# Kernel optimization log

Hardware: AMD Instinct MI355X
Metric: run time of the kernel (lower is better)

Reference implementation:

```python
import jax, jax.numpy as jnp
import numpy as np

NB = 8      # number of diagonal blocks per layer
BIN = 512   # in-block size
BOUT = 512  # out-block size


def setup_inputs() -> dict:
    key = jax.random.key(0)
    k_x, k_w1, k_b1, k_w2, k_b2 = jax.random.split(key, 5)
    B, D = 8192, NB * BIN
    x = jax.random.normal(k_x, (B, D), dtype=jnp.float32)
    # Block-diagonal weights stored as stacked blocks [NB, out_blk, in_blk]
    s1 = 1.0 / np.sqrt(BIN)
    W1 = jax.random.uniform(k_w1, (NB, BOUT, BIN), jnp.float32, -s1, s1)
    b1 = jax.random.uniform(k_b1, (NB * BOUT,), jnp.float32, -s1, s1)
    s2 = 1.0 / np.sqrt(BIN)
    W2 = jax.random.uniform(k_w2, (NB, BOUT, BIN), jnp.float32, -s2, s2)
    b2 = jax.random.uniform(k_b2, (NB * BOUT,), jnp.float32, -s2, s2)
    return {"x": x, "W1": W1, "b1": b1, "W2": W2, "b2": b2}


def _blockdiag_linear(x, W, b):
    # x: [B, NB*BIN]; W: [NB, BOUT, BIN]; b: [NB*BOUT]
    B = x.shape[0]
    xb = x.reshape(B, NB, BIN)                      # [B, NB, BIN]
    yb = jnp.einsum('bnc,noc->bno', xb, W)          # block-diag matmul
    return yb.reshape(B, NB * W.shape[1]) + b


def reference(x, W1, b1, W2, b2):
    x = x.reshape(x.shape[0], -1)                   # flatten(start_dim=1)
    h = jax.nn.relu(_blockdiag_linear(x, W1, b1))
    out = jax.nn.relu(_blockdiag_linear(h, W2, b2))
    return out
```

## Files before the change

kernel.cpp:

```cpp
#include <hip/hip_runtime.h>
#include <hip/hip_bf16.h>

#define NB 8
#define BIN 512
#define BOUT 512
#define BATCH 8192
#define DIM 4096

typedef __attribute__((ext_vector_type(8))) short bf16x8;
typedef __attribute__((ext_vector_type(4))) float f32x4;

#define SWZ(r) (((r) & 7) << 4)

__device__ __forceinline__ unsigned short f2bf(float f) {
    return __builtin_bit_cast(unsigned short, __float2bfloat16(f));
}

__device__ __forceinline__ unsigned long long pack4(f32x4 f) {
    return (unsigned long long)f2bf(f.x)
         | ((unsigned long long)f2bf(f.y) << 16)
         | ((unsigned long long)f2bf(f.z) << 32)
         | ((unsigned long long)f2bf(f.w) << 48);
}

__global__ void pack_w(const float* __restrict__ W, unsigned short* __restrict__ pk) {
    int gid = blockIdx.x * 256 + threadIdx.x;
    int lane = gid & 63;
    int n    = (gid >> 6) & 7;
    int kidx = (gid >> 9) & 15;
    int wn   = (gid >> 13) & 3;
    int nb   = gid >> 15;
    int row  = wn * 128 + n * 16 + (lane & 15);
    int col  = kidx * 32 + (lane >> 4) * 8;
    const float* s = W + ((size_t)nb * BOUT + row) * BIN + col;
    f32x4 a = *(const f32x4*)s;
    f32x4 b = *(const f32x4*)(s + 4);
    unsigned long long* d = (unsigned long long*)(pk + (size_t)gid * 8);
    d[0] = pack4(a);
    d[1] = pack4(b);
}

__global__ __launch_bounds__(256, 2)
void fused_mlp(const float* __restrict__ X,
               const unsigned short* __restrict__ PK1,
               const float* __restrict__ B1,
               const unsigned short* __restrict__ PK2,
               const float* __restrict__ B2,
               float* __restrict__ Out)
{
    __shared__ __align__(16) unsigned char LB[65536];

    const int bid = blockIdx.x;
    const int nb = bid & 7;
    const int mt = bid >> 3;

    const int t = threadIdx.x;
    const int lane = t & 63;
    const int wn = t >> 6;
    const int l15 = lane & 15;
    const int lhi = lane >> 4;

    const int row0 = mt * 64;
    const int wc0  = nb * 512;

    int ab[4][2];
    #pragma unroll
    for (int m = 0; m < 4; m++) {
        const int r_ = m * 16 + l15;
        #pragma unroll
        for (int par = 0; par < 2; par++)
            ab[m][par] = r_ * 1024 + ((par * 64 + lhi * 16) ^ SWZ(r_));
    }

    const unsigned short* wp1 = PK1 + (size_t)(nb * 4 + wn) * 65536 + lane * 8;
    const unsigned short* wp2 = PK2 + (size_t)(nb * 4 + wn) * 65536 + lane * 8;

    f32x4 acc[4][8];
    #pragma unroll
    for (int m = 0; m < 4; m++)
        #pragma unroll
        for (int n = 0; n < 8; n++)
            acc[m][n] = (f32x4)(0.f);

    bf16x8 q0[8], q1[8];

#define LOADQ(Q, WPTR) { \
    _Pragma("unroll") for (int n = 0; n < 8; n++) \
        Q[n] = *(const bf16x8*)((WPTR) + n * 512); \
    (WPTR) += 4096; }

#define MFMA32(Q, AF) \
    __builtin_amdgcn_s_setprio(1); \
    _Pragma("unroll") for (int m = 0; m < 4; m++) \
        _Pragma("unroll") for (int n = 0; n < 8; n++) \
            acc[m][n] = __builtin_amdgcn_mfma_f32_16x16x32_bf16(AF[m], Q[n], acc[m][n], 0, 0, 0); \
    __builtin_amdgcn_s_setprio(0);

#define HSTEP(QC, QN, WPTR, KIDX) { \
    LOADQ(QN, WPTR); \
    bf16x8 af[4]; \
    _Pragma("unroll") for (int m = 0; m < 4; m++) \
        af[m] = *(const bf16x8*)(LB + ab[m][(KIDX) & 1] + ((KIDX) >> 1) * 128); \
    MFMA32(QC, af) }

#define HSTEP_NL(QC, KIDX) { \
    bf16x8 af[4]; \
    _Pragma("unroll") for (int m = 0; m < 4; m++) \
        af[m] = *(const bf16x8*)(LB + ab[m][(KIDX) & 1] + ((KIDX) >> 1) * 128); \
    MFMA32(QC, af) }

#define BAR() { \
    asm volatile("s_waitcnt lgkmcnt(0)" ::: "memory"); \
    __builtin_amdgcn_s_barrier(); \
    __builtin_amdgcn_sched_barrier(0); }

    LOADQ(q0, wp1);

    {
        const int sr = t >> 2;
        const float* xr = X + (size_t)(row0 + sr) * DIM + wc0 + (t & 3) * 128;
        const int j0 = (t & 3) * 16;
        #pragma unroll
        for (int i = 0; i < 8; i++) {
            f32x4 a = *(const f32x4*)(xr + i * 16 + 0);
            f32x4 b = *(const f32x4*)(xr + i * 16 + 4);
            f32x4 c = *(const f32x4*)(xr + i * 16 + 8);
            f32x4 d = *(const f32x4*)(xr + i * 16 + 12);
            bf16x8 v0, v1;
            ((unsigned long long*)&v0)[0] = pack4(a);
            ((unsigned long long*)&v0)[1] = pack4(b);
            ((unsigned long long*)&v1)[0] = pack4(c);
            ((unsigned long long*)&v1)[1] = pack4(d);
            *(bf16x8*)(LB + sr * 1024 + (((j0 + 2 * i)     * 16) ^ SWZ(sr))) = v0;
            *(bf16x8*)(LB + sr * 1024 + (((j0 + 2 * i + 1) * 16) ^ SWZ(sr))) = v1;
        }
    }
    BAR();

    #pragma unroll
    for (int kp = 0; kp < 8; kp++) {
        HSTEP(q0, q1, wp1, 2 * kp);
        if (kp < 7) { HSTEP(q1, q0, wp1, 2 * kp + 1) }
        else        { HSTEP(q1, q0, wp2, 15)         }
    }

    BAR();

    #pragma unroll
    for (int n = 0; n < 8; n++) {
        const int c = wn * 128 + n * 16 + l15;
        const float bv = B1[wc0 + c];
        #pragma unroll
        for (int m = 0; m < 4; m++) {
            #pragma unroll
            for (int rr = 0; rr < 4; rr++) {
                float v = acc[m][n][rr] + bv;
                v = v > 0.f ? v : 0.f;
                const int r = m * 16 + lhi * 4 + rr;
                *(unsigned short*)(LB + r * 1024 + ((c * 2) ^ SWZ(r))) = f2bf(v);
            }
        }
    }
    BAR();

    #pragma unroll
    for (int m = 0; m < 4; m++)
        #pragma unroll
        for (int n = 0; n < 8; n++)
            acc[m][n] = (f32x4)(0.f);

    #pragma unroll
    for (int kp = 0; kp < 8; kp++) {
        HSTEP(q0, q1, wp2, 2 * kp);
        if (kp < 7) { HSTEP(q1, q0, wp2, 2 * kp + 1) }
        else        { HSTEP_NL(q1, 15) }
    }

    #pragma unroll
    for (int n = 0; n < 8; n++) {
        const int c = wc0 + wn * 128 + n * 16 + l15;
        const float bv = B2[c];
        #pragma unroll
        for (int m = 0; m < 4; m++) {
            const int rb = row0 + m * 16 + lhi * 4;
            #pragma unroll
            for (int rr = 0; rr < 4; rr++) {
                float v = acc[m][n][rr] + bv;
                Out[(size_t)(rb + rr) * DIM + c] = v > 0.f ? v : 0.f;
            }
        }
    }

#undef LOADQ
#undef MFMA32
#undef HSTEP
#undef HSTEP_NL
#undef BAR
}

extern "C" void kernel_launch(void* const* d_in, const int* in_sizes, int n_in,
                              void* d_out, int out_size, void* d_ws, size_t ws_size,
                              hipStream_t stream) {
    const float* x  = (const float*)d_in[0];
    const float* W1 = (const float*)d_in[1];
    const float* b1 = (const float*)d_in[2];
    const float* W2 = (const float*)d_in[3];
    const float* b2 = (const float*)d_in[4];
    float* out = (float*)d_out;

    char* ws = (char*)d_ws;
    unsigned short* PK1 = (unsigned short*)ws;
    unsigned short* PK2 = (unsigned short*)(ws + (4u << 20));

    pack_w<<<1024, 256, 0, stream>>>(W1, PK1);
    pack_w<<<1024, 256, 0, stream>>>(W2, PK2);

    const int GRID = NB * (BATCH / 64);
    fused_mlp<<<GRID, 256, 0, stream>>>(x, PK1, b1, PK2, b2, out);
}
```

Baseline: 101.5 us.

## Stage packed weights through triple-buffered LDS ring via async global_load_lds with 8 waves

Replaces per-wave register streaming of packed bf16 weights with a block-shared triple-buffered LDS ring filled by global_load_lds, synchronised by a vmcnt wait and barrier each k-step. The block grows to 512 threads with each wave owning 64 output columns, the weight packing layout is reordered to match, the X swizzle is widened to 16 rows, and biases are preloaded. The aim is to overlap weight fetch with MFMA work and cut register pressure. In exchange it adds a barrier per step, more A-fragment LDS reads per MFMA, and 160KB of LDS per block.

```diff
diff --git a/kernel.cpp b/kernel.cpp
--- a/kernel.cpp
+++ b/kernel.cpp
@@ -10,7 +10,7 @@
 typedef __attribute__((ext_vector_type(8))) short bf16x8;
 typedef __attribute__((ext_vector_type(4))) float f32x4;
 
-#define SWZ(r) (((r) & 7) << 4)
+#define SWZ16(r) (((r) & 15) << 4)
 
 __device__ __forceinline__ unsigned short f2bf(float f) {
     return __builtin_bit_cast(unsigned short, __float2bfloat16(f));
@@ -23,15 +23,21 @@
          | ((unsigned long long)f2bf(f.w) << 48);
 }
 
+__device__ __forceinline__ void gload16(const void* g, void* l) {
+    __builtin_amdgcn_global_load_lds(
+        (const __attribute__((address_space(1))) unsigned int*)g,
+        (__attribute__((address_space(3))) unsigned int*)l, 16, 0, 0);
+}
+
 __global__ void pack_w(const float* __restrict__ W, unsigned short* __restrict__ pk) {
     int gid = blockIdx.x * 256 + threadIdx.x;
     int lane = gid & 63;
-    int n    = (gid >> 6) & 7;
-    int kidx = (gid >> 9) & 15;
-    int wn   = (gid >> 13) & 3;
+    int s5   = (gid >> 6) & 31;
+    int kidx = (gid >> 11) & 15;
     int nb   = gid >> 15;
-    int row  = wn * 128 + n * 16 + (lane & 15);
-    int col  = kidx * 32 + (lane >> 4) * 8;
+    int wn = s5 >> 2, nf = s5 & 3;
+    int row = wn * 64 + nf * 16 + (lane & 15);
+    int col = kidx * 32 + (lane >> 4) * 8;
     const float* s = W + ((size_t)nb * BOUT + row) * BIN + col;
     f32x4 a = *(const f32x4*)s;
     f32x4 b = *(const f32x4*)(s + 4);
@@ -40,7 +46,7 @@
     d[1] = pack4(b);
 }
 
-__global__ __launch_bounds__(256, 2)
+__global__ __launch_bounds__(512, 2)
 void fused_mlp(const float* __restrict__ X,
                const unsigned short* __restrict__ PK1,
                const float* __restrict__ B1,
@@ -48,7 +54,9 @@
                const float* __restrict__ B2,
                float* __restrict__ Out)
 {
-    __shared__ __align__(16) unsigned char LB[65536];
+    __shared__ __align__(16) unsigned char POOL[163840];
+    unsigned char* XH = POOL;
+    unsigned char* RG = POOL + 65536;
 
     const int bid = blockIdx.x;
     const int nb = bid & 7;
@@ -56,108 +64,109 @@
 
     const int t = threadIdx.x;
     const int lane = t & 63;
-    const int wn = t >> 6;
+    const int wid = t >> 6;
     const int l15 = lane & 15;
     const int lhi = lane >> 4;
 
     const int row0 = mt * 64;
     const int wc0  = nb * 512;
 
-    int ab[4][2];
+    const unsigned short* pk1 = PK1 + (size_t)nb * 262144;
+    const unsigned short* pk2 = PK2 + (size_t)nb * 262144;
+
+    float bv1[4], bv2[4];
+    #pragma unroll
+    for (int n = 0; n < 4; n++) {
+        const int c = wc0 + wid * 64 + n * 16 + l15;
+        bv1[n] = B1[c];
+        bv2[n] = B2[c];
+    }
+
+    int ab[4][4];
     #pragma unroll
     for (int m = 0; m < 4; m++) {
         const int r_ = m * 16 + l15;
         #pragma unroll
-        for (int par = 0; par < 2; par++)
-            ab[m][par] = r_ * 1024 + ((par * 64 + lhi * 16) ^ SWZ(r_));
-    }
-
-    const unsigned short* wp1 = PK1 + (size_t)(nb * 4 + wn) * 65536 + lane * 8;
-    const unsigned short* wp2 = PK2 + (size_t)(nb * 4 + wn) * 65536 + lane * 8;
-
-    f32x4 acc[4][8];
+        for (int p = 0; p < 4; p++)
+            ab[m][p] = r_ * 1024 + ((p * 64 + lhi * 16) ^ SWZ16(r_));
+    }
+
+    const int wg_g = wid * 2048 + lane * 8;
+    const int wl_l = wid * 4096;
+    const int bptr = wid * 4096 + lane * 16;
+
+    f32x4 acc[4][4];
     #pragma unroll
     for (int m = 0; m < 4; m++)
         #pragma unroll
-        for (int n = 0; n < 8; n++)
+        for (int n = 0; n < 4; n++)
             acc[m][n] = (f32x4)(0.f);
 
-    bf16x8 q0[8], q1[8];
-
-#define LOADQ(Q, WPTR) { \
-    _Pragma("unroll") for (int n = 0; n < 8; n++) \
-        Q[n] = *(const bf16x8*)((WPTR) + n * 512); \
-    (WPTR) += 4096; }
-
-#define MFMA32(Q, AF) \
-    __builtin_amdgcn_s_setprio(1); \
-    _Pragma("unroll") for (int m = 0; m < 4; m++) \
-        _Pragma("unroll") for (int n = 0; n < 8; n++) \
-            acc[m][n] = __builtin_amdgcn_mfma_f32_16x16x32_bf16(AF[m], Q[n], acc[m][n], 0, 0, 0); \
-    __builtin_amdgcn_s_setprio(0);
-
-#define HSTEP(QC, QN, WPTR, KIDX) { \
-    LOADQ(QN, WPTR); \
-    bf16x8 af[4]; \
-    _Pragma("unroll") for (int m = 0; m < 4; m++) \
-        af[m] = *(const bf16x8*)(LB + ab[m][(KIDX) & 1] + ((KIDX) >> 1) * 128); \
-    MFMA32(QC, af) }
-
-#define HSTEP_NL(QC, KIDX) { \
-    bf16x8 af[4]; \
-    _Pragma("unroll") for (int m = 0; m < 4; m++) \
-        af[m] = *(const bf16x8*)(LB + ab[m][(KIDX) & 1] + ((KIDX) >> 1) * 128); \
-    MFMA32(QC, af) }
+#define ISSUE(G) { \
+    const unsigned short* tb_ = ((G) < 16 ? pk1 : pk2) + ((G) & 15) * 16384 + wg_g; \
+    unsigned char* lb_ = RG + ((G) % 3) * 32768 + wl_l; \
+    _Pragma("unroll") for (int i_ = 0; i_ < 4; i_++) \
+        gload16(tb_ + i_ * 512, lb_ + i_ * 1024); }
 
 #define BAR() { \
     asm volatile("s_waitcnt lgkmcnt(0)" ::: "memory"); \
     __builtin_amdgcn_s_barrier(); \
     __builtin_amdgcn_sched_barrier(0); }
 
-    LOADQ(q0, wp1);
-
+#define STEP(G) { \
+    if ((G) == 31) { asm volatile("s_waitcnt vmcnt(0)" ::: "memory"); } \
+    else           { asm volatile("s_waitcnt vmcnt(4)" ::: "memory"); } \
+    __builtin_amdgcn_s_barrier(); \
+    __builtin_amdgcn_sched_barrier(0); \
+    if ((G) + 2 <= 31) ISSUE((G) + 2); \
+    const unsigned char* wb_ = RG + ((G) % 3) * 32768; \
+    bf16x8 bfr[4]; \
+    _Pragma("unroll") for (int n_ = 0; n_ < 4; n_++) \
+        bfr[n_] = *(const bf16x8*)(wb_ + bptr + n_ * 1024); \
+    bf16x8 af[4]; \
+    const int kk_ = (G) & 15; \
+    _Pragma("unroll") for (int m_ = 0; m_ < 4; m_++) \
+        af[m_] = *(const bf16x8*)(XH + ab[m_][kk_ & 3] + (kk_ >> 2) * 256); \
+    __builtin_amdgcn_s_setprio(1); \
+    _Pragma("unroll") for (int m_ = 0; m_ < 4; m_++) \
+        _Pragma("unroll") for (int n_ = 0; n_ < 4; n_++) \
+            acc[m_][n_] = __builtin_amdgcn_mfma_f32_16x16x32_bf16(af[m_], bfr[n_], acc[m_][n_], 0, 0, 0); \
+    __builtin_amdgcn_s_setprio(0); }
+
+    ISSUE(0);
+    ISSUE(1);
     {
-        const int sr = t >> 2;
-        const float* xr = X + (size_t)(row0 + sr) * DIM + wc0 + (t & 3) * 128;
-        const int j0 = (t & 3) * 16;
+        const int sr = t >> 3;
+        const int c0 = (t & 7) * 64;
+        const float* xr = X + (size_t)(row0 + sr) * DIM + wc0 + c0;
         #pragma unroll
         for (int i = 0; i < 8; i++) {
-            f32x4 a = *(const f32x4*)(xr + i * 16 + 0);
-            f32x4 b = *(const f32x4*)(xr + i * 16 + 4);
-            f32x4 c = *(const f32x4*)(xr + i * 16 + 8);
-            f32x4 d = *(const f32x4*)(xr + i * 16 + 12);
-            bf16x8 v0, v1;
-            ((unsigned long long*)&v0)[0] = pack4(a);
-            ((unsigned long long*)&v0)[1] = pack4(b);
-            ((unsigned long long*)&v1)[0] = pack4(c);
-            ((unsigned long long*)&v1)[1] = pack4(d);
-            *(bf16x8*)(LB + sr * 1024 + (((j0 + 2 * i)     * 16) ^ SWZ(sr))) = v0;
-            *(bf16x8*)(LB + sr * 1024 + (((j0 + 2 * i + 1) * 16) ^ SWZ(sr))) = v1;
+            f32x4 a = *(const f32x4*)(xr + i * 8);
+            f32x4 b = *(const f32x4*)(xr + i * 8 + 4);
+            bf16x8 v;
+            ((unsigned long long*)&v)[0] = pack4(a);
+            ((unsigned long long*)&v)[1] = pack4(b);
+            *(bf16x8*)(XH + sr * 1024 + ((((c0 + i * 8) * 2)) ^ SWZ16(sr))) = v;
         }
     }
     BAR();
 
     #pragma unroll
-    for (int kp = 0; kp < 8; kp++) {
-        HSTEP(q0, q1, wp1, 2 * kp);
-        if (kp < 7) { HSTEP(q1, q0, wp1, 2 * kp + 1) }
-        else        { HSTEP(q1, q0, wp2, 15)         }
-    }
+    for (int g = 0; g < 16; g++) STEP(g);
 
     BAR();
 
     #pragma unroll
-    for (int n = 0; n < 8; n++) {
-        const int c = wn * 128 + n * 16 + l15;
-        const float bv = B1[wc0 + c];
+    for (int n = 0; n < 4; n++) {
+        const int c = wid * 64 + n * 16 + l15;
         #pragma unroll
         for (int m = 0; m < 4; m++) {
             #pragma unroll
             for (int rr = 0; rr < 4; rr++) {
-                float v = acc[m][n][rr] + bv;
+                float v = acc[m][n][rr] + bv1[n];
                 v = v > 0.f ? v : 0.f;
                 const int r = m * 16 + lhi * 4 + rr;
-                *(unsigned short*)(LB + r * 1024 + ((c * 2) ^ SWZ(r))) = f2bf(v);
+                *(unsigned short*)(XH + r * 1024 + ((c * 2) ^ SWZ16(r))) = f2bf(v);
             }
         }
     }
@@ -166,36 +175,29 @@
     #pragma unroll
     for (int m = 0; m < 4; m++)
         #pragma unroll
-        for (int n = 0; n < 8; n++)
+        for (int n = 0; n < 4; n++)
             acc[m][n] = (f32x4)(0.f);
 
     #pragma unroll
-    for (int kp = 0; kp < 8; kp++) {
-        HSTEP(q0, q1, wp2, 2 * kp);
-        if (kp < 7) { HSTEP(q1, q0, wp2, 2 * kp + 1) }
-        else        { HSTEP_NL(q1, 15) }
-    }
-
-    #pragma unroll
-    for (int n = 0; n < 8; n++) {
-        const int c = wc0 + wn * 128 + n * 16 + l15;
-        const float bv = B2[c];
+    for (int g = 16; g < 32; g++) STEP(g);
+
+    #pragma unroll
+    for (int n = 0; n < 4; n++) {
+        const int c = wc0 + wid * 64 + n * 16 + l15;
         #pragma unroll
         for (int m = 0; m < 4; m++) {
             const int rb = row0 + m * 16 + lhi * 4;
             #pragma unroll
             for (int rr = 0; rr < 4; rr++) {
-                float v = acc[m][n][rr] + bv;
+                float v = acc[m][n][rr] + bv2[n];
                 Out[(size_t)(rb + rr) * DIM + c] = v > 0.f ? v : 0.f;
             }
         }
     }
 
-#undef LOADQ
-#undef MFMA32
-#undef HSTEP
-#undef HSTEP_NL
+#undef ISSUE
 #undef BAR
+#undef STEP
 }
 
 extern "C" void kernel_launch(void* const* d_in, const int* in_sizes, int n_in,
@@ -216,5 +218,5 @@
     pack_w<<<1024, 256, 0, stream>>>(W2, PK2);
 
     const int GRID = NB * (BATCH / 64);
-    fused_mlp<<<GRID, 256, 0, stream>>>(x, PK1, b1, PK2, b2, out);
-}
+    fused_mlp<<<GRID, 512, 0, stream>>>(x, PK1, b1, PK2, b2, out);
+}
```

After: 121.1 us. 1.19x slower.
